# Performance work log

Measured on AMD Instinct MI355X. Metric: run time of the kernel, lower is better.

## Reference

```python
import jax, jax.numpy as jnp
import numpy as np

EMBED = 256
HID = EMBED * 4
NUM_EXPERTS = 4
WINDOW = 16
B, T = 4, 4096
EPS = 1e-5


def _ln(x, g, b):
    m = jnp.mean(x, axis=-1, keepdims=True)
    v = jnp.mean(jnp.square(x - m), axis=-1, keepdims=True)
    return (x - m) / jnp.sqrt(v + EPS) * g + b


def setup_inputs() -> dict:
    key = jax.random.key(0)
    ks = jax.random.split(key, 16)
    s = 0.02
    d = {
        'x': jax.random.normal(ks[0], (B, T, EMBED), jnp.float32),
        'ln1_g': jnp.ones((EMBED,), jnp.float32),
        'ln1_b': jnp.zeros((EMBED,), jnp.float32),
        'qkv_w': jax.random.normal(ks[1], (EMBED, 3 * EMBED), jnp.float32) * s,
        'qkv_b': jnp.zeros((3 * EMBED,), jnp.float32),
        'proj_w': jax.random.normal(ks[2], (EMBED, EMBED), jnp.float32) * s,
        'proj_b': jnp.zeros((EMBED,), jnp.float32),
        'attn_gate': jnp.ones((EMBED,), jnp.float32),
        'ln2_g': jnp.ones((EMBED,), jnp.float32),
        'ln2_b': jnp.zeros((EMBED,), jnp.float32),
        'gating_w': jax.random.normal(ks[3], (EMBED, NUM_EXPERTS), jnp.float32) * s,
        'gating_b': jnp.zeros((NUM_EXPERTS,), jnp.float32),
        'e_w1': jax.random.normal(ks[4], (NUM_EXPERTS, EMBED, HID), jnp.float32) * s,
        'e_b1': jnp.zeros((NUM_EXPERTS, HID), jnp.float32),
        'e_w2': jax.random.normal(ks[5], (NUM_EXPERTS, HID, EMBED), jnp.float32) * s,
        'e_b2': jnp.zeros((NUM_EXPERTS, EMBED), jnp.float32),
    }
    return d


def reference(x, ln1_g, ln1_b, qkv_w, qkv_b, proj_w, proj_b, attn_gate,
              ln2_g, ln2_b, gating_w, gating_b, e_w1, e_b1, e_w2, e_b2):
    Bx, Tx, C = x.shape
    # --- sparse attention branch ---
    h = _ln(x, ln1_g, ln1_b)
    qkv = h @ qkv_w + qkv_b                      # [B,T,3C]
    q, k, v = jnp.split(qkv, 3, axis=-1)
    scores = jnp.einsum('btc,bsc->bts', q, k) / jnp.sqrt(jnp.float32(C))
    idx = jnp.arange(Tx)
    diff = idx[:, None] - idx[None, :]           # i - j
    in_window = (diff >= 0) & (diff <= WINDOW)
    # faithful to torch code: scores outside the window (but causal) stay 0,
    # positions above the diagonal become -inf; softmax over full row
    scores = jnp.where(in_window, scores, 0.0)
    scores = jnp.where(diff >= 0, scores, -jnp.inf)
    att = jax.nn.softmax(scores, axis=-1)        # [B,T,T]
    a_out = jnp.einsum('bts,bsc->btc', att, v) * attn_gate
    x = x + a_out @ proj_w + proj_b
    # --- dense all-expert MoE branch ---
    h2 = _ln(x, ln2_g, ln2_b)
    gates = jax.nn.softmax(h2 @ gating_w + gating_b, axis=-1)     # [B,T,E]
    hid = jax.nn.gelu(jnp.einsum('btc,ech->bteh', h2, e_w1) + e_b1,
                      approximate=False)                           # [B,T,E,H]
    eo = jnp.einsum('bteh,eho->bteo', hid, e_w2) + e_b2            # [B,T,E,C]
    moe_out = jnp.einsum('bte,bteo->bto', gates, eo)
    return x + moe_out
```

## Files before the change

kernel.cpp:

```cpp
#include <hip/hip_runtime.h>
#include <hip/hip_bf16.h>
#include <math.h>

#define T_   4096
#define B_   4
#define C_   256
#define C3_  768
#define H_   1024
#define E_   4
#define M_   (B_*T_)
#define NCH_ 64
#define CHL_ (T_/NCH_)
#define KH_  4096

typedef __attribute__((ext_vector_type(8))) short short8;
typedef __attribute__((ext_vector_type(4))) float floatx4;

__device__ __forceinline__ float b2f(unsigned short u) {
  union { unsigned int i; float f; } x; x.i = ((unsigned int)u) << 16; return x.f;
}
__device__ __forceinline__ unsigned short f2b(float f) {
  __hip_bfloat16 h = __float2bfloat16(f);
  return *reinterpret_cast<unsigned short*>(&h);
}
__device__ __forceinline__ void unpack8(uint4 a, float* f) {
  unsigned int w[4] = {a.x, a.y, a.z, a.w};
  #pragma unroll
  for (int i = 0; i < 4; i++) {
    union { unsigned int u; float g; } lo, hi;
    lo.u = w[i] << 16; hi.u = w[i] & 0xffff0000u;
    f[2*i] = lo.g; f[2*i+1] = hi.g;
  }
}
__device__ __forceinline__ void gl_lds16(const void* g, void* l) {
  __builtin_amdgcn_global_load_lds(
      (const __attribute__((address_space(1))) void*)g,
      (__attribute__((address_space(3))) void*)l, 16, 0, 0);
}
__device__ __forceinline__ float gelu_s(float v) {
  float e = __expf(-1.702f * v);
  return v * __builtin_amdgcn_rcpf(1.0f + e);
}
__device__ __forceinline__ unsigned int pk_fp8x4(float a, float b, float c, float d) {
  unsigned int v = 0;
  v = __builtin_amdgcn_cvt_pk_fp8_f32(a, b, v, false);
  v = __builtin_amdgcn_cvt_pk_fp8_f32(c, d, v, true);
  return v;
}
__device__ __forceinline__ unsigned char f2fp8(float v) {
  return (unsigned char)(__builtin_amdgcn_cvt_pk_fp8_f32(v, v, 0, false) & 0xff);
}
__device__ __forceinline__ float sel4(float4 v, int e) {
  float r = v.x;
  r = (e == 1) ? v.y : r;
  r = (e == 2) ? v.z : r;
  r = (e == 3) ? v.w : r;
  return r;
}

__global__ __launch_bounds__(256) void transpose_cvt(
    const float* __restrict__ src, unsigned short* __restrict__ dst, int K, int N,
    int dstLd, size_t dstZStride) {
  __shared__ float tile[32][33];
  src += (size_t)blockIdx.z * K * N;
  dst += (size_t)blockIdx.z * dstZStride;
  int n0 = blockIdx.x * 32, k0 = blockIdx.y * 32;
  int tx = threadIdx.x, ty = threadIdx.y;
  #pragma unroll
  for (int i = 0; i < 32; i += 8)
    tile[ty + i][tx] = src[(size_t)(k0 + ty + i) * N + n0 + tx];
  __syncthreads();
  #pragma unroll
  for (int i = 0; i < 32; i += 8)
    dst[(size_t)(n0 + ty + i) * dstLd + k0 + tx] = f2b(tile[tx][ty + i]);
}

__global__ __launch_bounds__(256) void transpose_w2_fp8(
    const float* __restrict__ src, unsigned char* __restrict__ dst) {
  __shared__ float tile[32][33];
  int e = blockIdx.z;
  src += (size_t)e * H_ * C_;
  int h0 = blockIdx.x * 32, c0 = blockIdx.y * 32;
  int tx = threadIdx.x, ty = threadIdx.y;
  #pragma unroll
  for (int i = 0; i < 32; i += 8)
    tile[ty + i][tx] = src[(size_t)(h0 + ty + i) * C_ + c0 + tx];
  __syncthreads();
  int k = e * H_ + h0 + tx;
  int chunk = k >> 6, kc = k & 63;
  #pragma unroll
  for (int i = 0; i < 32; i += 8) {
    int c = c0 + ty + i;
    int sw = ((((kc >> 4) ^ (c & 3)) << 4) | (kc & 15));
    dst[((size_t)chunk * 256 + c) * 64 + sw] = f2fp8(tile[tx][ty + i] * 256.0f);
  }
}

__global__ __launch_bounds__(256) void ln1_kernel(
    const float* __restrict__ x, const float* __restrict__ g,
    const float* __restrict__ b, unsigned short* __restrict__ h) {
  __shared__ float red[4];
  int row = blockIdx.x, tid = threadIdx.x;
  float v = x[(size_t)row * C_ + tid];
  float s = v;
  #pragma unroll
  for (int o = 32; o; o >>= 1) s += __shfl_xor(s, o);
  if ((tid & 63) == 0) red[tid >> 6] = s;
  __syncthreads();
  float mean = (red[0] + red[1] + red[2] + red[3]) * (1.0f / C_);
  __syncthreads();
  float d = v - mean;
  float q = d * d;
  #pragma unroll
  for (int o = 32; o; o >>= 1) q += __shfl_xor(q, o);
  if ((tid & 63) == 0) red[tid >> 6] = q;
  __syncthreads();
  float var = (red[0] + red[1] + red[2] + red[3]) * (1.0f / C_);
  h[(size_t)row * C_ + tid] = f2b(d * rsqrtf(var + 1e-5f) * g[tid] + b[tid]);
}

__global__ __launch_bounds__(256) void ln2_gates_kernel(
    const float* __restrict__ x1, const float* __restrict__ g,
    const float* __restrict__ b, const float* __restrict__ gw,
    const float* __restrict__ gb, unsigned short* __restrict__ h2,
    float* __restrict__ gates) {
  __shared__ float red[4];
  __shared__ float redg[4][4];
  int row = blockIdx.x, tid = threadIdx.x;
  float v = x1[(size_t)row * C_ + tid];
  float s = v;
  #pragma unroll
  for (int o = 32; o; o >>= 1) s += __shfl_xor(s, o);
  if ((tid & 63) == 0) red[tid >> 6] = s;
  __syncthreads();
  float mean = (red[0] + red[1] + red[2] + red[3]) * (1.0f / C_);
  __syncthreads();
  float d = v - mean;
  float q = d * d;
  #pragma unroll
  for (int o = 32; o; o >>= 1) q += __shfl_xor(q, o);
  if ((tid & 63) == 0) red[tid >> 6] = q;
  __syncthreads();
  float var = (red[0] + red[1] + red[2] + red[3]) * (1.0f / C_);
  float hv = d * rsqrtf(var + 1e-5f) * g[tid] + b[tid];
  h2[(size_t)row * C_ + tid] = f2b(hv);
  float p0 = hv * gw[tid * 4 + 0];
  float p1 = hv * gw[tid * 4 + 1];
  float p2 = hv * gw[tid * 4 + 2];
  float p3 = hv * gw[tid * 4 + 3];
  #pragma unroll
  for (int o = 32; o; o >>= 1) {
    p0 += __shfl_xor(p0, o); p1 += __shfl_xor(p1, o);
    p2 += __shfl_xor(p2, o); p3 += __shfl_xor(p3, o);
  }
  if ((tid & 63) == 0) {
    int w = tid >> 6;
    redg[w][0] = p0; redg[w][1] = p1; redg[w][2] = p2; redg[w][3] = p3;
  }
  __syncthreads();
  if (tid == 0) {
    float t4[4];
    #pragma unroll
    for (int e = 0; e < 4; e++)
      t4[e] = redg[0][e] + redg[1][e] + redg[2][e] + redg[3][e] + gb[e];
    float m = fmaxf(fmaxf(t4[0], t4[1]), fmaxf(t4[2], t4[3]));
    float zs = 0.f;
    #pragma unroll
    for (int e = 0; e < 4; e++) { t4[e] = __expf(t4[e] - m); zs += t4[e]; }
    float inv = 1.0f / zs;
    #pragma unroll
    for (int e = 0; e < 4; e++) gates[(size_t)row * 4 + e] = t4[e] * inv;
  }
}

__global__ __launch_bounds__(256) void scan1_kernel(const unsigned short* __restrict__ qkv,
                                                    float* __restrict__ S) {
  int b = blockIdx.x >> 6, ch = blockIdx.x & 63, c = threadIdx.x;
  float s = 0.f;
  size_t base = ((size_t)b * T_ + (size_t)ch * CHL_) * C3_ + 512 + c;
  for (int t = 0; t < CHL_; t++) s += b2f(qkv[base + (size_t)t * C3_]);
  S[((size_t)b * NCH_ + ch) * C_ + c] = s;
}
__global__ __launch_bounds__(256) void scan2_kernel(float* __restrict__ S) {
  int b = blockIdx.x, c = threadIdx.x;
  float run = 0.f;
  for (int ch = 0; ch < NCH_; ch++) {
    size_t i = ((size_t)b * NCH_ + ch) * C_ + c;
    float t = S[i]; S[i] = run; run += t;
  }
}
__global__ __launch_bounds__(256) void scan3_kernel(const unsigned short* __restrict__ qkv,
                                                    const float* __restrict__ S,
                                                    unsigned short* __restrict__ Pb) {
  int b = blockIdx.x >> 6, ch = blockIdx.x & 63, c = threadIdx.x;
  float run = S[((size_t)b * NCH_ + ch) * C_ + c];
  size_t row0 = (size_t)b * T_ + (size_t)ch * CHL_;
  for (int t = 0; t < CHL_; t++) {
    run += b2f(qkv[(row0 + t) * C3_ + 512 + c]);
    Pb[(row0 + t) * C_ + c] = f2b(run);
  }
}

__global__ __launch_bounds__(256) void attn_kernel(
    const unsigned short* __restrict__ qkv, const unsigned short* __restrict__ Pb,
    const float* __restrict__ gate, unsigned short* __restrict__ aout) {
  int wave = threadIdx.x >> 6, lane = threadIdx.x & 63;
  int r = blockIdx.x * 4 + wave;
  int t = r & (T_ - 1);
  int g = lane >> 4, u = lane & 15;
  const unsigned short* qp = qkv + (size_t)r * C3_ + (u << 4);
  float qv[16];
  unpack8(*(const uint4*)qp, qv);
  unpack8(*(const uint4*)(qp + 8), qv + 8);
  float sc[5];
  #pragma unroll
  for (int rnd = 0; rnd < 5; rnd++) {
    int j = rnd * 4 + g;
    int jj = t - 16 + j;
    bool valid = (j <= 16) && (jj >= 0);
    float d = 0.f;
    if (valid) {
      const unsigned short* kp = qkv + (size_t)(r - 16 + j) * C3_ + 256 + (u << 4);
      float kv[16];
      unpack8(*(const uint4*)kp, kv);
      unpack8(*(const uint4*)(kp + 8), kv + 8);
      #pragma unroll
      for (int c = 0; c < 16; c++) d += qv[c] * kv[c];
    }
    d += __shfl_xor(d, 1); d += __shfl_xor(d, 2);
    d += __shfl_xor(d, 4); d += __shfl_xor(d, 8);
    sc[rnd] = valid ? d * 0.0625f : -1e30f;
  }
  float m = fmaxf(fmaxf(fmaxf(sc[0], sc[1]), fmaxf(sc[2], sc[3])), sc[4]);
  m = fmaxf(m, __shfl_xor(m, 16));
  m = fmaxf(m, __shfl_xor(m, 32));
  if (t > 16) m = fmaxf(m, 0.0f);
  float ev[5], Zp = 0.f;
  #pragma unroll
  for (int rnd = 0; rnd < 5; rnd++) {
    ev[rnd] = (sc[rnd] > -1e29f) ? __expf(sc[rnd] - m) : 0.f;
    Zp += ev[rnd];
  }
  Zp += __shfl_xor(Zp, 16);
  Zp += __shfl_xor(Zp, 32);
  float e0v = 0.f;
  if (t > 16) { e0v = __expf(-m); Zp += e0v * (float)(t - 16); }
  float vp[16];
  #pragma unroll
  for (int c = 0; c < 16; c++) vp[c] = 0.f;
  #pragma unroll
  for (int rnd = 0; rnd < 5; rnd++) {
    if (ev[rnd] != 0.f) {
      int j = rnd * 4 + g;
      const unsigned short* vpp = qkv + (size_t)(r - 16 + j) * C3_ + 512 + (u << 4);
      float vv[16];
      unpack8(*(const uint4*)vpp, vv);
      unpack8(*(const uint4*)(vpp + 8), vv + 8);
      #pragma unroll
      for (int c = 0; c < 16; c++) vp[c] += ev[rnd] * vv[c];
    }
  }
  #pragma unroll
  for (int c = 0; c < 16; c++) {
    vp[c] += __shfl_xor(vp[c], 16);
    vp[c] += __shfl_xor(vp[c], 32);
  }
  if (g == 0) {
    if (t > 16) {
      const unsigned short* pp = Pb + (size_t)(r - 17) * C_ + (u << 4);
      float pv[16];
      unpack8(*(const uint4*)pp, pv);
      unpack8(*(const uint4*)(pp + 8), pv + 8);
      #pragma unroll
      for (int c = 0; c < 16; c++) vp[c] += e0v * pv[c];
    }
    float inv = 1.0f / Zp;
    const float* gp = gate + (u << 4);
    unsigned int ow[8];
    #pragma unroll
    for (int i = 0; i < 8; i++) {
      unsigned short lo = f2b(vp[2*i] * inv * gp[2*i]);
      unsigned short hi = f2b(vp[2*i+1] * inv * gp[2*i+1]);
      ow[i] = (unsigned int)lo | ((unsigned int)hi << 16);
    }
    uint4 s0 = {ow[0], ow[1], ow[2], ow[3]};
    uint4 s1 = {ow[4], ow[5], ow[6], ow[7]};
    *(uint4*)(aout + (size_t)r * C_ + (u << 4)) = s0;
    *(uint4*)(aout + (size_t)r * C_ + (u << 4) + 8) = s1;
  }
}

template<int EPI>
__global__ __launch_bounds__(256) void gemm128(
    const unsigned short* __restrict__ A, const unsigned short* __restrict__ Bt,
    const float* __restrict__ bias, int K, int ldOut,
    const float* __restrict__ resid, float* __restrict__ outf,
    unsigned short* __restrict__ outb) {
  __shared__ __align__(16) unsigned short As[128 * 64];
  __shared__ __align__(16) unsigned short Bs[128 * 64];
  const int tid = threadIdx.x;
  const int wave = tid >> 6, lane = tid & 63;
  const int mBlk = blockIdx.x * 128, nBlk = blockIdx.y * 128;
  const int wm = (wave >> 1) * 64, wn = (wave & 1) * 64;
  const int lm = lane & 15, lk = (lane >> 4) * 8;
  floatx4 acc[4][4];
  #pragma unroll
  for (int i = 0; i < 4; i++)
    #pragma unroll
    for (int j = 0; j < 4; j++) acc[i][j] = (floatx4){0.f, 0.f, 0.f, 0.f};

  for (int kt = 0; kt < K; kt += 64) {
    __syncthreads();
    #pragma unroll
    for (int i = 0; i < 4; i++) {
      int seg = i * 256 + tid;
      int row = seg >> 3, g = seg & 7;
      int gc = (g ^ (row & 7)) << 3;
      gl_lds16(A + (size_t)(mBlk + row) * K + kt + gc, &As[seg * 8]);
      gl_lds16(Bt + (size_t)(nBlk + row) * K + kt + gc, &Bs[seg * 8]);
    }
    __syncthreads();
    #pragma unroll
    for (int kk = 0; kk < 64; kk += 32) {
      short8 mf[4], nf[4];
      #pragma unroll
      for (int j = 0; j < 4; j++) {
        int row = wm + j * 16 + lm;
        mf[j] = *(const short8*)&As[row * 64 + ((((kk + lk) >> 3) ^ (row & 7)) << 3)];
      }
      #pragma unroll
      for (int i = 0; i < 4; i++) {
        int row = wn + i * 16 + lm;
        nf[i] = *(const short8*)&Bs[row * 64 + ((((kk + lk) >> 3) ^ (row & 7)) << 3)];
      }
      #pragma unroll
      for (int i = 0; i < 4; i++)
        #pragma unroll
        for (int j = 0; j < 4; j++)
          acc[i][j] = __builtin_amdgcn_mfma_f32_16x16x32_bf16(nf[i], mf[j], acc[i][j], 0, 0, 0);
    }
  }
  const int lc = lane & 15, quad = lane >> 4, q4 = quad * 4;
  #pragma unroll
  for (int i = 0; i < 4; i++) {
    int n0 = nBlk + wn + i * 16 + q4;
    float4 bs = *(const float4*)&bias[n0];
    #pragma unroll
    for (int j = 0; j < 4; j++) {
      int m = mBlk + wm + j * 16 + lc;
      float v0 = acc[i][j][0] + bs.x, v1 = acc[i][j][1] + bs.y;
      float v2 = acc[i][j][2] + bs.z, v3 = acc[i][j][3] + bs.w;
      if (EPI == 0) {
        ushort4 o = {f2b(v0), f2b(v1), f2b(v2), f2b(v3)};
        *(ushort4*)&outb[(size_t)m * ldOut + n0] = o;
      } else {
        size_t idx = (size_t)m * ldOut + n0;
        float4 r = *(const float4*)&resid[idx];
        float4 o = {v0 + r.x, v1 + r.y, v2 + r.z, v3 + r.w};
        *(float4*)&outf[idx] = o;
      }
    }
  }
}

__global__ __launch_bounds__(256, 1) void moe_fused(
    const unsigned short* __restrict__ h2,
    const unsigned short* __restrict__ w1t,
    const float* __restrict__ b1,
    const unsigned char* __restrict__ w2b,
    const float* __restrict__ b2,
    const float* __restrict__ gates,
    const float* __restrict__ x1,
    float* __restrict__ out) {
  __shared__ __align__(16) unsigned short As[64 * 256];
  __shared__ __align__(16) unsigned short W1s[2][64 * 256];
  __shared__ __align__(16) unsigned char  W2s[2][256 * 64];
  __shared__ __align__(16) unsigned char  Hs[64 * 64];
  __shared__ __align__(16) float          B1s[2][64];
  const int tid = threadIdx.x;
  const int wave = tid >> 6, lane = tid & 63;
  const int lm = lane & 15, quad = lane >> 4;
  const int mb = blockIdx.x * 64;
  const int wmu = (wave >> 1) * 32;
  const int whu = (wave & 1) * 32;
  const int wc  = wave * 64;

  #pragma unroll
  for (int t = 0; t < 8; t++) {
    int seg = t * 256 + tid;
    int row = seg >> 5, g = seg & 31;
    int gp = (g & 24) | ((g & 7) ^ (row & 7));
    gl_lds16(h2 + (size_t)(mb + row) * C_ + gp * 8, &As[seg * 8]);
  }

  auto stageW = [&](int c, int buf) {
    const unsigned short* ws = w1t + (size_t)c * 64 * C_;
    #pragma unroll
    for (int t = 0; t < 8; t++) {
      int seg = t * 256 + tid;
      int row = seg >> 5, g = seg & 31;
      int gp = (g & 24) | ((g & 7) ^ (row & 7));
      gl_lds16(ws + (size_t)row * C_ + gp * 8, &W1s[buf][seg * 8]);
    }
    const unsigned char* vs = w2b + (size_t)c * 256 * 64;
    #pragma unroll
    for (int t = 0; t < 4; t++) {
      int seg = t * 256 + tid;
      gl_lds16(vs + (size_t)seg * 16, &W2s[buf][seg * 16]);
    }
    if (lane < 16)
      gl_lds16(b1 + (size_t)c * 64 + lane * 4, &B1s[buf][0]);
  };

  stageW(0, 0);

  float4 ga[2];
  #pragma unroll
  for (int j = 0; j < 2; j++)
    ga[j] = *(const float4*)(gates + (size_t)(mb + wmu + j * 16 + lm) * 4);

  floatx4 dacc[4][4];
  #pragma unroll
  for (int i = 0; i < 4; i++)
    #pragma unroll
    for (int j = 0; j < 4; j++) dacc[i][j] = (floatx4){0.f, 0.f, 0.f, 0.f};

  asm volatile("s_waitcnt vmcnt(0)" ::: "memory");
  __builtin_amdgcn_s_barrier();
  __builtin_amdgcn_sched_barrier(0);

  for (int c = 0; c < 64; c++) {
    const int cb = c & 1;
    __builtin_amdgcn_s_barrier();
    __builtin_amdgcn_sched_barrier(0);
    stageW((c + 1) & 63, cb ^ 1);
    asm volatile("s_waitcnt vmcnt(13)" ::: "memory");
    __builtin_amdgcn_s_barrier();
    __builtin_amdgcn_sched_barrier(0);

    floatx4 uacc[2][2];
    #pragma unroll
    for (int i = 0; i < 2; i++)
      #pragma unroll
      for (int j = 0; j < 2; j++) uacc[i][j] = (floatx4){0.f, 0.f, 0.f, 0.f};
    #pragma unroll
    for (int kk = 0; kk < 8; kk++) {
      int kc = kk * 4 + quad;
      short8 mf[2], nf[2];
      #pragma unroll
      for (int j = 0; j < 2; j++) {
        int row = wmu + j * 16 + lm;
        mf[j] = *(const short8*)&As[row * 256 + ((kc ^ (row & 7)) << 3)];
      }
      #pragma unroll
      for (int i = 0; i < 2; i++) {
        int row = whu + i * 16 + lm;
        nf[i] = *(const short8*)&W1s[cb][row * 256 + ((kc ^ (row & 7)) << 3)];
      }
      #pragma unroll
      for (int i = 0; i < 2; i++)
        #pragma unroll
        for (int j = 0; j < 2; j++)
          uacc[i][j] = __builtin_amdgcn_mfma_f32_16x16x32_bf16(nf[i], mf[j], uacc[i][j], 0, 0, 0);
    }

    int e = c >> 4;
    float gs0 = 64.0f * sel4(ga[0], e);
    float gs1 = 64.0f * sel4(ga[1], e);
    #pragma unroll
    for (int i = 0; i < 2; i++) {
      float4 bb = *(const float4*)&B1s[cb][whu + i * 16 + quad * 4];
      #pragma unroll
      for (int j = 0; j < 2; j++) {
        float gs = j ? gs1 : gs0;
        unsigned int w = pk_fp8x4(gs * gelu_s(uacc[i][j][0] + bb.x),
                                  gs * gelu_s(uacc[i][j][1] + bb.y),
                                  gs * gelu_s(uacc[i][j][2] + bb.z),
                                  gs * gelu_s(uacc[i][j][3] + bb.w));
        int m = wmu + j * 16 + lm;
        int hh = whu + i * 16 + quad * 4;
        *(unsigned int*)&Hs[m * 64 + ((((hh >> 3) ^ (m & 7)) << 3) | (hh & 7))] = w;
      }
    }
    asm volatile("s_waitcnt lgkmcnt(0)" ::: "memory");
    __builtin_amdgcn_s_barrier();
    __builtin_amdgcn_sched_barrier(0);

    #pragma unroll
    for (int kk = 0; kk < 2; kk++) {
      long mfh[4], nfw[4];
      #pragma unroll
      for (int j = 0; j < 4; j++) {
        int m = j * 16 + lm;
        int g8 = quad + 4 * kk;
        mfh[j] = *(const long*)&Hs[m * 64 + ((g8 ^ (m & 7)) << 3)];
      }
      #pragma unroll
      for (int i = 0; i < 4; i++) {
        int cr = wc + i * 16 + lm;
        int sl = ((quad >> 1) + 2 * kk) ^ (cr & 3);
        nfw[i] = *(const long*)&W2s[cb][cr * 64 + (sl << 4) + ((quad & 1) << 3)];
      }
      #pragma unroll
      for (int i = 0; i < 4; i++)
        #pragma unroll
        for (int j = 0; j < 4; j++)
          dacc[i][j] = __builtin_amdgcn_mfma_f32_16x16x32_fp8_fp8(nfw[i], mfh[j], dacc[i][j], 0, 0, 0);
    }
  }

  const float sc = 1.0f / 16384.0f;
  const int q4 = quad * 4;
  #pragma unroll
  for (int j = 0; j < 4; j++) {
    int m = mb + j * 16 + lm;
    float4 g4 = *(const float4*)(gates + (size_t)m * 4);
    #pragma unroll
    for (int i = 0; i < 4; i++) {
      int n0 = wc + i * 16 + q4;
      float4 bA = *(const float4*)&b2[0 * C_ + n0];
      float4 bB = *(const float4*)&b2[1 * C_ + n0];
      float4 bC = *(const float4*)&b2[2 * C_ + n0];
      float4 bD = *(const float4*)&b2[3 * C_ + n0];
      size_t idx = (size_t)m * C_ + n0;
      float4 r = *(const float4*)&x1[idx];
      float4 o;
      o.x = dacc[i][j][0]*sc + r.x + g4.x*bA.x + g4.y*bB.x + g4.z*bC.x + g4.w*bD.x;
      o.y = dacc[i][j][1]*sc + r.y + g4.x*bA.y + g4.y*bB.y + g4.z*bC.y + g4.w*bD.y;
      o.z = dacc[i][j][2]*sc + r.z + g4.x*bA.z + g4.y*bB.z + g4.z*bC.z + g4.w*bD.z;
      o.w = dacc[i][j][3]*sc + r.w + g4.x*bA.w + g4.y*bB.w + g4.z*bC.w + g4.w*bD.w;
      *(float4*)&out[idx] = o;
    }
  }
}

extern "C" void kernel_launch(void* const* d_in, const int* in_sizes, int n_in,
                              void* d_out, int out_size, void* d_ws, size_t ws_size,
                              hipStream_t stream) {
  const float* x       = (const float*)d_in[0];
  const float* ln1_g   = (const float*)d_in[1];
  const float* ln1_b   = (const float*)d_in[2];
  const float* qkv_w   = (const float*)d_in[3];
  const float* qkv_b   = (const float*)d_in[4];
  const float* proj_w  = (const float*)d_in[5];
  const float* proj_b  = (const float*)d_in[6];
  const float* attn_g  = (const float*)d_in[7];
  const float* ln2_g   = (const float*)d_in[8];
  const float* ln2_b   = (const float*)d_in[9];
  const float* gat_w   = (const float*)d_in[10];
  const float* gat_b   = (const float*)d_in[11];
  const float* e_w1    = (const float*)d_in[12];
  const float* e_b1    = (const float*)d_in[13];
  const float* e_w2    = (const float*)d_in[14];
  const float* e_b2    = (const float*)d_in[15];
  float* out = (float*)d_out;

  char* p = (char*)d_ws;
  unsigned short* h    = (unsigned short*)p; p += (size_t)M_ * C_ * 2;
  unsigned short* qkv  = (unsigned short*)p; p += (size_t)M_ * C3_ * 2;
  unsigned short* Pb   = (unsigned short*)p; p += (size_t)M_ * C_ * 2;
  unsigned short* aout = (unsigned short*)p; p += (size_t)M_ * C_ * 2;
  float*          x1   = (float*)p;          p += (size_t)M_ * C_ * 4;
  unsigned short* h2   = (unsigned short*)p; p += (size_t)M_ * C_ * 2;
  float*          gts  = (float*)p;          p += (size_t)M_ * E_ * 4;
  float*          S    = (float*)p;          p += (size_t)B_ * NCH_ * C_ * 4;
  unsigned short* wq   = (unsigned short*)p; p += (size_t)C3_ * C_ * 2;
  unsigned short* wp   = (unsigned short*)p; p += (size_t)C_ * C_ * 2;
  unsigned short* w1t  = (unsigned short*)p; p += (size_t)KH_ * C_ * 2;
  unsigned char*  w2f8 = (unsigned char*)p;  p += (size_t)C_ * KH_;

  dim3 t32x8(32, 8);
  transpose_cvt<<<dim3(C3_/32, C_/32, 1), t32x8, 0, stream>>>(qkv_w, wq, C_, C3_, C_, 0);
  transpose_cvt<<<dim3(C_/32, C_/32, 1),  t32x8, 0, stream>>>(proj_w, wp, C_, C_, C_, 0);
  transpose_cvt<<<dim3(H_/32, C_/32, E_), t32x8, 0, stream>>>(e_w1, w1t, C_, H_, C_, (size_t)H_ * C_);
  transpose_w2_fp8<<<dim3(H_/32, C_/32, E_), t32x8, 0, stream>>>(e_w2, w2f8);

  ln1_kernel<<<M_, 256, 0, stream>>>(x, ln1_g, ln1_b, h);
  gemm128<0><<<dim3(M_/128, C3_/128), 256, 0, stream>>>(h, wq, qkv_b, C_, C3_,
      nullptr, nullptr, qkv);
  scan1_kernel<<<B_*NCH_, 256, 0, stream>>>(qkv, S);
  scan2_kernel<<<B_, 256, 0, stream>>>(S);
  scan3_kernel<<<B_*NCH_, 256, 0, stream>>>(qkv, S, Pb);
  attn_kernel<<<M_/4, 256, 0, stream>>>(qkv, Pb, attn_g, aout);
  gemm128<1><<<dim3(M_/128, C_/128), 256, 0, stream>>>(aout, wp, proj_b, C_, C_,
      x, x1, nullptr);
  ln2_gates_kernel<<<M_, 256, 0, stream>>>(x1, ln2_g, ln2_b, gat_w, gat_b, h2, gts);
  moe_fused<<<M_/64, 256, 0, stream>>>(h2, w1t, e_b1, w2f8, e_b2, gts, x1, out);
}
```

Measured before the change: 348.4 us.

## Warp-specialize MoE kernel into up-proj and down-proj wave groups with pipelined H

Doubles the MoE block to 512 threads and splits it into four up-projection waves and four down-projection waves, with the down waves working on the previous chunk's hidden tile through a double-buffered Hs. The up waves keep their h2 A-fragments in registers instead of LDS, which frees the As buffer and lets two blocks share a CU. The aim is to overlap the bf16 up GEMM and GELU with the fp8 down GEMM and to raise occupancy. The cost is more register pressure from the 16 held A fragments, a 512-thread block bound with 2 blocks per CU, and waits that must stay correct for the new vmcnt accounting.

```diff
diff --git a/kernel.cpp b/kernel.cpp
--- a/kernel.cpp
+++ b/kernel.cpp
@@ -363,7 +363,7 @@
   }
 }
 
-__global__ __launch_bounds__(256, 1) void moe_fused(
+__global__ __launch_bounds__(512, 2) void moe_fused(
     const unsigned short* __restrict__ h2,
     const unsigned short* __restrict__ w1t,
     const float* __restrict__ b1,
@@ -372,120 +372,146 @@
     const float* __restrict__ gates,
     const float* __restrict__ x1,
     float* __restrict__ out) {
-  __shared__ __align__(16) unsigned short As[64 * 256];
   __shared__ __align__(16) unsigned short W1s[2][64 * 256];
   __shared__ __align__(16) unsigned char  W2s[2][256 * 64];
-  __shared__ __align__(16) unsigned char  Hs[64 * 64];
+  __shared__ __align__(16) unsigned char  Hs[2][64 * 64];
   __shared__ __align__(16) float          B1s[2][64];
   const int tid = threadIdx.x;
   const int wave = tid >> 6, lane = tid & 63;
   const int lm = lane & 15, quad = lane >> 4;
   const int mb = blockIdx.x * 64;
-  const int wmu = (wave >> 1) * 32;
-  const int whu = (wave & 1) * 32;
-  const int wc  = wave * 64;
-
-  #pragma unroll
-  for (int t = 0; t < 8; t++) {
-    int seg = t * 256 + tid;
-    int row = seg >> 5, g = seg & 31;
-    int gp = (g & 24) | ((g & 7) ^ (row & 7));
-    gl_lds16(h2 + (size_t)(mb + row) * C_ + gp * 8, &As[seg * 8]);
-  }
-
-  auto stageW = [&](int c, int buf) {
+  const bool isUp = wave < 4;
+  const int uw = wave & 3;
+  const int wmu = (uw >> 1) * 32;
+  const int whu = (uw & 1) * 32;
+  const int wc  = uw * 64;
+
+  auto stageW1 = [&](int c, int buf) {
     const unsigned short* ws = w1t + (size_t)c * 64 * C_;
     #pragma unroll
-    for (int t = 0; t < 8; t++) {
-      int seg = t * 256 + tid;
+    for (int t = 0; t < 4; t++) {
+      int seg = t * 512 + tid;
       int row = seg >> 5, g = seg & 31;
       int gp = (g & 24) | ((g & 7) ^ (row & 7));
       gl_lds16(ws + (size_t)row * C_ + gp * 8, &W1s[buf][seg * 8]);
     }
-    const unsigned char* vs = w2b + (size_t)c * 256 * 64;
-    #pragma unroll
-    for (int t = 0; t < 4; t++) {
-      int seg = t * 256 + tid;
-      gl_lds16(vs + (size_t)seg * 16, &W2s[buf][seg * 16]);
-    }
     if (lane < 16)
       gl_lds16(b1 + (size_t)c * 64 + lane * 4, &B1s[buf][0]);
   };
-
-  stageW(0, 0);
-
+  auto stageW2 = [&](int c, int buf) {
+    const unsigned char* vs = w2b + (size_t)c * 256 * 64;
+    #pragma unroll
+    for (int t = 0; t < 2; t++) {
+      int seg = t * 512 + tid;
+      gl_lds16(vs + (size_t)seg * 16, &W2s[buf][seg * 16]);
+    }
+  };
+
+  stageW1(0, 0);
+
+  short8 af[8][2];
   float4 ga[2];
-  #pragma unroll
-  for (int j = 0; j < 2; j++)
-    ga[j] = *(const float4*)(gates + (size_t)(mb + wmu + j * 16 + lm) * 4);
+  if (isUp) {
+    #pragma unroll
+    for (int kk = 0; kk < 8; kk++) {
+      int kc = kk * 4 + quad;
+      #pragma unroll
+      for (int j = 0; j < 2; j++) {
+        int row = mb + wmu + j * 16 + lm;
+        af[kk][j] = *(const short8*)(h2 + (size_t)row * C_ + kc * 8);
+      }
+    }
+    #pragma unroll
+    for (int j = 0; j < 2; j++)
+      ga[j] = *(const float4*)(gates + (size_t)(mb + wmu + j * 16 + lm) * 4);
+  }
 
   floatx4 dacc[4][4];
   #pragma unroll
   for (int i = 0; i < 4; i++)
     #pragma unroll
     for (int j = 0; j < 4; j++) dacc[i][j] = (floatx4){0.f, 0.f, 0.f, 0.f};
+
+  for (int c = 0; c < 64; c++) {
+    const int wb = c & 1;
+    __builtin_amdgcn_s_barrier();
+    __builtin_amdgcn_sched_barrier(0);
+    stageW1((c + 1) & 63, wb ^ 1);
+    stageW2(c, wb);
+    asm volatile("s_waitcnt vmcnt(7)" ::: "memory");
+    __builtin_amdgcn_s_barrier();
+    __builtin_amdgcn_sched_barrier(0);
+
+    if (isUp) {
+      floatx4 uacc[2][2];
+      #pragma unroll
+      for (int i = 0; i < 2; i++)
+        #pragma unroll
+        for (int j = 0; j < 2; j++) uacc[i][j] = (floatx4){0.f, 0.f, 0.f, 0.f};
+      #pragma unroll
+      for (int kk = 0; kk < 8; kk++) {
+        int kc = kk * 4 + quad;
+        short8 nf[2];
+        #pragma unroll
+        for (int i = 0; i < 2; i++) {
+          int row = whu + i * 16 + lm;
+          nf[i] = *(const short8*)&W1s[wb][row * 256 + ((kc ^ (row & 7)) << 3)];
+        }
+        #pragma unroll
+        for (int i = 0; i < 2; i++)
+          #pragma unroll
+          for (int j = 0; j < 2; j++)
+            uacc[i][j] = __builtin_amdgcn_mfma_f32_16x16x32_bf16(nf[i], af[kk][j], uacc[i][j], 0, 0, 0);
+      }
+      int e = c >> 4;
+      float gs0 = 64.0f * sel4(ga[0], e);
+      float gs1 = 64.0f * sel4(ga[1], e);
+      #pragma unroll
+      for (int i = 0; i < 2; i++) {
+        float4 bb = *(const float4*)&B1s[wb][whu + i * 16 + quad * 4];
+        #pragma unroll
+        for (int j = 0; j < 2; j++) {
+          float gs = j ? gs1 : gs0;
+          unsigned int w = pk_fp8x4(gs * gelu_s(uacc[i][j][0] + bb.x),
+                                    gs * gelu_s(uacc[i][j][1] + bb.y),
+                                    gs * gelu_s(uacc[i][j][2] + bb.z),
+                                    gs * gelu_s(uacc[i][j][3] + bb.w));
+          int m = wmu + j * 16 + lm;
+          int hh = whu + i * 16 + quad * 4;
+          *(unsigned int*)&Hs[wb][m * 64 + ((((hh >> 3) ^ (m & 7)) << 3) | (hh & 7))] = w;
+        }
+      }
+      asm volatile("s_waitcnt lgkmcnt(0)" ::: "memory");
+    } else if (c > 0) {
+      const int pb = wb ^ 1;
+      #pragma unroll
+      for (int kk = 0; kk < 2; kk++) {
+        long mfh[4], nfw[4];
+        #pragma unroll
+        for (int j = 0; j < 4; j++) {
+          int m = j * 16 + lm;
+          int g8 = quad + 4 * kk;
+          mfh[j] = *(const long*)&Hs[pb][m * 64 + ((g8 ^ (m & 7)) << 3)];
+        }
+        #pragma unroll
+        for (int i = 0; i < 4; i++) {
+          int cr = wc + i * 16 + lm;
+          int sl = ((quad >> 1) + 2 * kk) ^ (cr & 3);
+          nfw[i] = *(const long*)&W2s[pb][cr * 64 + (sl << 4) + ((quad & 1) << 3)];
+        }
+        #pragma unroll
+        for (int i = 0; i < 4; i++)
+          #pragma unroll
+          for (int j = 0; j < 4; j++)
+            dacc[i][j] = __builtin_amdgcn_mfma_f32_16x16x32_fp8_fp8(nfw[i], mfh[j], dacc[i][j], 0, 0, 0);
+      }
+    }
+  }
 
   asm volatile("s_waitcnt vmcnt(0)" ::: "memory");
   __builtin_amdgcn_s_barrier();
   __builtin_amdgcn_sched_barrier(0);
-
-  for (int c = 0; c < 64; c++) {
-    const int cb = c & 1;
-    __builtin_amdgcn_s_barrier();
-    __builtin_amdgcn_sched_barrier(0);
-    stageW((c + 1) & 63, cb ^ 1);
-    asm volatile("s_waitcnt vmcnt(13)" ::: "memory");
-    __builtin_amdgcn_s_barrier();
-    __builtin_amdgcn_sched_barrier(0);
-
-    floatx4 uacc[2][2];
-    #pragma unroll
-    for (int i = 0; i < 2; i++)
-      #pragma unroll
-      for (int j = 0; j < 2; j++) uacc[i][j] = (floatx4){0.f, 0.f, 0.f, 0.f};
-    #pragma unroll
-    for (int kk = 0; kk < 8; kk++) {
-      int kc = kk * 4 + quad;
-      short8 mf[2], nf[2];
-      #pragma unroll
-      for (int j = 0; j < 2; j++) {
-        int row = wmu + j * 16 + lm;
-        mf[j] = *(const short8*)&As[row * 256 + ((kc ^ (row & 7)) << 3)];
-      }
-      #pragma unroll
-      for (int i = 0; i < 2; i++) {
-        int row = whu + i * 16 + lm;
-        nf[i] = *(const short8*)&W1s[cb][row * 256 + ((kc ^ (row & 7)) << 3)];
-      }
-      #pragma unroll
-      for (int i = 0; i < 2; i++)
-        #pragma unroll
-        for (int j = 0; j < 2; j++)
-          uacc[i][j] = __builtin_amdgcn_mfma_f32_16x16x32_bf16(nf[i], mf[j], uacc[i][j], 0, 0, 0);
-    }
-
-    int e = c >> 4;
-    float gs0 = 64.0f * sel4(ga[0], e);
-    float gs1 = 64.0f * sel4(ga[1], e);
-    #pragma unroll
-    for (int i = 0; i < 2; i++) {
-      float4 bb = *(const float4*)&B1s[cb][whu + i * 16 + quad * 4];
-      #pragma unroll
-      for (int j = 0; j < 2; j++) {
-        float gs = j ? gs1 : gs0;
-        unsigned int w = pk_fp8x4(gs * gelu_s(uacc[i][j][0] + bb.x),
-                                  gs * gelu_s(uacc[i][j][1] + bb.y),
-                                  gs * gelu_s(uacc[i][j][2] + bb.z),
-                                  gs * gelu_s(uacc[i][j][3] + bb.w));
-        int m = wmu + j * 16 + lm;
-        int hh = whu + i * 16 + quad * 4;
-        *(unsigned int*)&Hs[m * 64 + ((((hh >> 3) ^ (m & 7)) << 3) | (hh & 7))] = w;
-      }
-    }
-    asm volatile("s_waitcnt lgkmcnt(0)" ::: "memory");
-    __builtin_amdgcn_s_barrier();
-    __builtin_amdgcn_sched_barrier(0);
-
+  if (!isUp) {
     #pragma unroll
     for (int kk = 0; kk < 2; kk++) {
       long mfh[4], nfw[4];
@@ -493,13 +519,13 @@
       for (int j = 0; j < 4; j++) {
         int m = j * 16 + lm;
         int g8 = quad + 4 * kk;
-        mfh[j] = *(const long*)&Hs[m * 64 + ((g8 ^ (m & 7)) << 3)];
+        mfh[j] = *(const long*)&Hs[1][m * 64 + ((g8 ^ (m & 7)) << 3)];
       }
       #pragma unroll
       for (int i = 0; i < 4; i++) {
         int cr = wc + i * 16 + lm;
         int sl = ((quad >> 1) + 2 * kk) ^ (cr & 3);
-        nfw[i] = *(const long*)&W2s[cb][cr * 64 + (sl << 4) + ((quad & 1) << 3)];
+        nfw[i] = *(const long*)&W2s[1][cr * 64 + (sl << 4) + ((quad & 1) << 3)];
       }
       #pragma unroll
       for (int i = 0; i < 4; i++)
@@ -507,29 +533,28 @@
         for (int j = 0; j < 4; j++)
           dacc[i][j] = __builtin_amdgcn_mfma_f32_16x16x32_fp8_fp8(nfw[i], mfh[j], dacc[i][j], 0, 0, 0);
     }
-  }
-
-  const float sc = 1.0f / 16384.0f;
-  const int q4 = quad * 4;
-  #pragma unroll
-  for (int j = 0; j < 4; j++) {
-    int m = mb + j * 16 + lm;
-    float4 g4 = *(const float4*)(gates + (size_t)m * 4);
-    #pragma unroll
-    for (int i = 0; i < 4; i++) {
-      int n0 = wc + i * 16 + q4;
-      float4 bA = *(const float4*)&b2[0 * C_ + n0];
-      float4 bB = *(const float4*)&b2[1 * C_ + n0];
-      float4 bC = *(const float4*)&b2[2 * C_ + n0];
-      float4 bD = *(const float4*)&b2[3 * C_ + n0];
-      size_t idx = (size_t)m * C_ + n0;
-      float4 r = *(const float4*)&x1[idx];
-      float4 o;
-      o.x = dacc[i][j][0]*sc + r.x + g4.x*bA.x + g4.y*bB.x + g4.z*bC.x + g4.w*bD.x;
-      o.y = dacc[i][j][1]*sc + r.y + g4.x*bA.y + g4.y*bB.y + g4.z*bC.y + g4.w*bD.y;
-      o.z = dacc[i][j][2]*sc + r.z + g4.x*bA.z + g4.y*bB.z + g4.z*bC.z + g4.w*bD.z;
-      o.w = dacc[i][j][3]*sc + r.w + g4.x*bA.w + g4.y*bB.w + g4.z*bC.w + g4.w*bD.w;
-      *(float4*)&out[idx] = o;
+    const float sc = 1.0f / 16384.0f;
+    const int q4 = quad * 4;
+    #pragma unroll
+    for (int j = 0; j < 4; j++) {
+      int m = mb + j * 16 + lm;
+      float4 g4 = *(const float4*)(gates + (size_t)m * 4);
+      #pragma unroll
+      for (int i = 0; i < 4; i++) {
+        int n0 = wc + i * 16 + q4;
+        float4 bA = *(const float4*)&b2[0 * C_ + n0];
+        float4 bB = *(const float4*)&b2[1 * C_ + n0];
+        float4 bC = *(const float4*)&b2[2 * C_ + n0];
+        float4 bD = *(const float4*)&b2[3 * C_ + n0];
+        size_t idx = (size_t)m * C_ + n0;
+        float4 r = *(const float4*)&x1[idx];
+        float4 o;
+        o.x = dacc[i][j][0]*sc + r.x + g4.x*bA.x + g4.y*bB.x + g4.z*bC.x + g4.w*bD.x;
+        o.y = dacc[i][j][1]*sc + r.y + g4.x*bA.y + g4.y*bB.y + g4.z*bC.y + g4.w*bD.y;
+        o.z = dacc[i][j][2]*sc + r.z + g4.x*bA.z + g4.y*bB.z + g4.z*bC.z + g4.w*bD.z;
+        o.w = dacc[i][j][3]*sc + r.w + g4.x*bA.w + g4.y*bB.w + g4.z*bC.w + g4.w*bD.w;
+        *(float4*)&out[idx] = o;
+      }
     }
   }
 }
@@ -585,5 +610,5 @@
   gemm128<1><<<dim3(M_/128, C_/128), 256, 0, stream>>>(aout, wp, proj_b, C_, C_,
       x, x1, nullptr);
   ln2_gates_kernel<<<M_, 256, 0, stream>>>(x1, ln2_g, ln2_b, gat_w, gat_b, h2, gts);
-  moe_fused<<<M_/64, 256, 0, stream>>>(h2, w1t, e_b1, w2f8, e_b2, gts, x1, out);
-}
+  moe_fused<<<M_/64, 512, 0, stream>>>(h2, w1t, e_b1, w2f8, e_b2, gts, x1, out);
+}
```

Measured after the change: 320.4 us. 1.09x faster.
